# Performance work log

Measured on AMD Instinct MI355X. Metric: run time of the kernel, lower is better.

Reference implementation:

```python
import jax, jax.numpy as jnp
import numpy as np

N_NODES = 5000
N_EDGES = 50000
HIDDEN = 64
EDGE_DIM = 16


def setup_inputs() -> dict:
    key = jax.random.key(0)
    ks = jax.random.split(key, 8)
    d = HIDDEN
    h = jax.random.normal(ks[0], (N_NODES, d), dtype=jnp.float32)
    edge_index = jax.random.randint(ks[1], (2, N_EDGES), 0, N_NODES, dtype=jnp.int64)
    edge_features = jax.random.normal(ks[2], (N_EDGES, EDGE_DIM), dtype=jnp.float32)
    # edge-network MLP: Linear(edge_dim, d) -> ReLU -> Linear(d, d*d)
    W1 = jax.random.normal(ks[3], (EDGE_DIM, d), dtype=jnp.float32) * (1.0 / np.sqrt(EDGE_DIM))
    b1 = jnp.zeros((d,), dtype=jnp.float32)
    W2 = jax.random.normal(ks[4], (d, d * d), dtype=jnp.float32) * (1.0 / np.sqrt(d))
    b2 = jnp.zeros((d * d,), dtype=jnp.float32)
    # GRUCell params (torch layout: rows = [reset; update; new])
    W_ih = jax.random.normal(ks[5], (3 * d, d), dtype=jnp.float32) * (1.0 / np.sqrt(d))
    W_hh = jax.random.normal(ks[6], (3 * d, d), dtype=jnp.float32) * (1.0 / np.sqrt(d))
    b_ih = jnp.zeros((3 * d,), dtype=jnp.float32)
    b_hh = jnp.zeros((3 * d,), dtype=jnp.float32)
    return {"h": h, "edge_index": edge_index, "edge_features": edge_features,
            "W1": W1, "b1": b1, "W2": W2, "b2": b2,
            "W_ih": W_ih, "W_hh": W_hh, "b_ih": b_ih, "b_hh": b_hh}


def reference(h, edge_index, edge_features, W1, b1, W2, b2, W_ih, W_hh, b_ih, b_hh):
    n_nodes, d = h.shape
    src, tgt = edge_index[0], edge_index[1]
    # 1) gather sender states
    h_w = h[src]  # (E, d)
    # 2-3) edge MLP -> per-edge transformation matrices (E, d, d)
    A = jax.nn.relu(edge_features @ W1 + b1) @ W2 + b2
    A = A.reshape(-1, d, d)
    # 4) per-edge matvec messages
    msg = jnp.einsum('eij,ej->ei', A, h_w)  # (E, d)
    # 5) scatter-sum aggregation per target node
    m = jax.ops.segment_sum(msg, tgt, num_segments=n_nodes)  # (N, d)
    # 6) GRUCell(m, h) - torch semantics
    gi = m @ W_ih.T + b_ih   # (N, 3d)
    gh = h @ W_hh.T + b_hh   # (N, 3d)
    i_r, i_z, i_n = jnp.split(gi, 3, axis=-1)
    h_r, h_z, h_n = jnp.split(gh, 3, axis=-1)
    r = jax.nn.sigmoid(i_r + h_r)
    z = jax.nn.sigmoid(i_z + h_z)
    n = jnp.tanh(i_n + r * h_n)
    h_new = (1.0 - z) * n + z * h
    return h_new
```

## Files before the change

kernel.cpp:

```cpp
#include <hip/hip_runtime.h>
#include <math.h>

#define N_NODES 5000
#define N_EDGES 50000
#define NPAD 5008
#define KP 4224
#define KSPLIT 3
#define POISON_I ((int)0xAAAAAAAAu)

typedef _Float16 f16x8 __attribute__((ext_vector_type(8)));
typedef _Float16 f16x2 __attribute__((ext_vector_type(2)));
typedef float    f32x4 __attribute__((ext_vector_type(4)));

static __device__ __forceinline__ f32x4 mfma16f(f16x8 a, f16x8 b, f32x4 c) {
    return __builtin_amdgcn_mfma_f32_16x16x32_f16(a, b, c, 0, 0, 0);
}

__global__ void prep_kernel(const float* __restrict__ W2, const float* __restrict__ b2,
                            const float* __restrict__ Wih, const float* __restrict__ Whh,
                            const int* __restrict__ ei,
                            _Float16* __restrict__ Br, float* __restrict__ WihT,
                            float* __restrict__ WhhT, int* __restrict__ cnt) {
    int g = blockIdx.x * 256 + threadIdx.x;
    if (g < 33792) {
        int nt = g / 8448, rem = g - nt * 8448;
        int ks = rem >> 6, lane = rem & 63;
        int lo = lane & 15, q = lane >> 4;
        int i = nt * 16 + lo, kap0 = ks * 32 + q * 8;
        f16x8 v;
#pragma unroll
        for (int p = 0; p < 8; ++p) {
            int kap = kap0 + p;
            int k2 = kap >> 7, rem2 = kap & 127;
            int j = rem2 >> 1, k = k2 * 2 + (rem2 & 1);
            float x = 0.f;
            if (k < 64) x = W2[(size_t)k * 4096 + i * 64 + j];
            else if (k == 64) x = b2[i * 64 + j];
            v[p] = (_Float16)x;
        }
        *(f16x8*)(Br + (size_t)g * 8) = v;
        return;
    }
    g -= 33792;
    if (g < 24576) {
        int which = g >= 12288;
        int tt = which ? g - 12288 : g;
        int row = tt >> 6, j = tt & 63;
        (which ? WhhT : WihT)[j * 192 + row] = (which ? Whh : Wih)[tt];
        return;
    }
    g -= 24576;
    if (g < N_EDGES) atomicAdd(&cnt[ei[N_EDGES + g]], 1);
}

__global__ __launch_bounds__(1024) void scan_kernel(const int* __restrict__ cnt,
                                                    int* __restrict__ off,
                                                    int* __restrict__ cur) {
    __shared__ int s[1024];
    int tid = threadIdx.x;
    int base = tid * 5;
    int loc[5]; int sum = 0;
#pragma unroll
    for (int q = 0; q < 5; ++q) {
        int v = (base + q < N_NODES) ? (cnt[base + q] - POISON_I) : 0;
        loc[q] = sum; sum += v;
    }
    s[tid] = sum; __syncthreads();
    for (int d = 1; d < 1024; d <<= 1) {
        int v = (tid >= d) ? s[tid - d] : 0;
        __syncthreads();
        s[tid] += v;
        __syncthreads();
    }
    int excl = (tid > 0) ? s[tid - 1] : 0;
#pragma unroll
    for (int q = 0; q < 5; ++q)
        if (base + q < N_NODES) { off[base + q] = excl + loc[q]; cur[base + q] = excl + loc[q]; }
    if (tid == 1023) off[N_NODES] = excl + sum;
}

__global__ void scatter_kernel(const int* __restrict__ ei, int* __restrict__ cur,
                               int* __restrict__ srcp, int* __restrict__ eidp) {
    int e = blockIdx.x * 256 + threadIdx.x;
    if (e < N_EDGES) {
        int q = atomicAdd(&cur[ei[N_EDGES + e]], 1);
        srcp[q] = ei[e];
        eidp[q] = e;
    }
}

__global__ __launch_bounds__(256) void hbuild_kernel(const int* __restrict__ toff,
                                                     const int* __restrict__ srcp,
                                                     const int* __restrict__ eidp,
                                                     const float* __restrict__ ef,
                                                     const float* __restrict__ W1,
                                                     const float* __restrict__ b1,
                                                     const float* __restrict__ h,
                                                     _Float16* __restrict__ H) {
    __shared__ float tls[16][64];
    __shared__ float hls[16][64];
    int tid = threadIdx.x, kc = tid >> 6, lane = tid & 63;
    int v = blockIdx.x;
    float acc[16];
#pragma unroll
    for (int k = 0; k < 16; ++k) acc[k] = 0.f;
    float acc64 = 0.f;
    int s0 = 0, s1 = 0;
    if (v < N_NODES) { s0 = toff[v]; s1 = toff[v + 1]; }
    float w1c[16];
#pragma unroll
    for (int k = 0; k < 16; ++k) w1c[k] = W1[k * 64 + lane];
    float b1l = b1[lane];
    for (int tb = s0; tb < s1; tb += 16) {
        int tcnt = s1 - tb; if (tcnt > 16) tcnt = 16;
        int eidx[4], sidx[4];
#pragma unroll
        for (int r = 0; r < 4; ++r) {
            int idx = kc * 4 + r;
            if (idx < tcnt) {
                eidx[r] = eidp[tb + idx];
                sidx[r] = srcp[tb + idx];
            }
        }
#pragma unroll
        for (int r = 0; r < 4; ++r) {
            int idx = kc * 4 + r;
            if (idx < tcnt) {
                hls[idx][lane] = h[(size_t)sidx[r] * 64 + lane];
                const float* efr = ef + (size_t)eidx[r] * 16;
                float tacc = b1l;
#pragma unroll
                for (int k = 0; k < 16; ++k) tacc += efr[k] * w1c[k];
                tls[idx][lane] = fmaxf(tacc, 0.f);
            }
        }
        __syncthreads();
        int q = 0;
        for (; q + 1 < tcnt; q += 2) {
            float hv0 = hls[q][lane];
            float hv1 = hls[q + 1][lane];
            const float4* t0 = (const float4*)&tls[q][kc * 16];
            const float4* t1 = (const float4*)&tls[q + 1][kc * 16];
#pragma unroll
            for (int b = 0; b < 4; ++b) {
                float4 a = t0[b], c = t1[b];
                acc[b * 4 + 0] += a.x * hv0; acc[b * 4 + 0] += c.x * hv1;
                acc[b * 4 + 1] += a.y * hv0; acc[b * 4 + 1] += c.y * hv1;
                acc[b * 4 + 2] += a.z * hv0; acc[b * 4 + 2] += c.z * hv1;
                acc[b * 4 + 3] += a.w * hv0; acc[b * 4 + 3] += c.w * hv1;
            }
            acc64 += hv0 + hv1;
        }
        if (q < tcnt) {
            float hv = hls[q][lane];
            const float4* t0 = (const float4*)&tls[q][kc * 16];
#pragma unroll
            for (int b = 0; b < 4; ++b) {
                float4 a = t0[b];
                acc[b * 4 + 0] += a.x * hv;
                acc[b * 4 + 1] += a.y * hv;
                acc[b * 4 + 2] += a.z * hv;
                acc[b * 4 + 3] += a.w * hv;
            }
            acc64 += hv;
        }
        __syncthreads();
    }
    _Float16* Hv = H + (size_t)v * KP;
#pragma unroll
    for (int p = 0; p < 8; ++p) {
        f16x2 pv = { (_Float16)acc[p * 2], (_Float16)acc[p * 2 + 1] };
        *(f16x2*)(Hv + (kc * 8 + p) * 128 + lane * 2) = pv;
    }
    if (kc == 3) {
        f16x2 pv = { (_Float16)acc64, (_Float16)0.f };
        *(f16x2*)(Hv + 32 * 128 + lane * 2) = pv;
    }
}

__global__ __launch_bounds__(256) void gemm_part(const _Float16* __restrict__ H,
                                                 const _Float16* __restrict__ Br,
                                                 float* __restrict__ gp) {
    __shared__ _Float16 As[2][16 * 136];
    int tid = threadIdx.x, w = tid >> 6, lane = tid & 63;
    int lo = lane & 15, q = lane >> 4;
    int m0 = blockIdx.x * 16;
    int ksp = blockIdx.y;
    int ar = tid >> 4, ac = (tid & 15) * 8;
    const _Float16* Ag = H + (size_t)(m0 + ar) * KP + ksp * 1408 + ac;
    f32x4 acc = {0.f, 0.f, 0.f, 0.f};
    f16x8 pf = *(const f16x8*)(Ag);
    *(f16x8*)(&As[0][ar * 136 + ac]) = pf;
    __syncthreads();
    for (int c = 0; c < 11; ++c) {
        if (c + 1 < 11) pf = *(const f16x8*)(Ag + (size_t)(c + 1) * 128);
        const _Float16* Arow = &As[c & 1][lo * 136];
        int ksg = (ksp * 11 + c) * 4;
#pragma unroll
        for (int ks = 0; ks < 4; ++ks) {
            f16x8 a = *(const f16x8*)(Arow + ks * 32 + q * 8);
            f16x8 b = *(const f16x8*)(Br + ((size_t)((w * 132 + ksg + ks) * 64 + lane)) * 8);
            acc = mfma16f(a, b, acc);
        }
        if (c + 1 < 11) *(f16x8*)(&As[(c + 1) & 1][ar * 136 + ac]) = pf;
        __syncthreads();
    }
    float* gpo = gp + (size_t)ksp * NPAD * 64;
    int row4 = q * 4;
#pragma unroll
    for (int g = 0; g < 4; ++g)
        gpo[(size_t)(m0 + row4 + g) * 64 + w * 16 + lo] = acc[g];
}

__global__ void gru_kernel(const float* __restrict__ gp,
                           const float* __restrict__ h,
                           const float* __restrict__ WihT,
                           const float* __restrict__ WhhT,
                           const float* __restrict__ bih,
                           const float* __restrict__ bhh,
                           float* __restrict__ out) {
    int w = threadIdx.x >> 6, lane = threadIdx.x & 63;
    int n = blockIdx.x * 4 + w;
    int i = lane;
    float ir = bih[i], iz = bih[64 + i], inn = bih[128 + i];
    float hr = bhh[i], hz = bhh[64 + i], hn = bhh[128 + i];
    const float4* g0 = (const float4*)(gp + (size_t)n * 64);
    const float4* g1 = (const float4*)(gp + (size_t)NPAD * 64 + (size_t)n * 64);
    const float4* g2 = (const float4*)(gp + (size_t)2 * NPAD * 64 + (size_t)n * 64);
    const float4* hnp = (const float4*)(h + (size_t)n * 64);
#pragma unroll 4
    for (int qb = 0; qb < 16; ++qb) {
        float4 a = g0[qb], b = g1[qb], c = g2[qb];
        float4 hv = hnp[qb];
        float mj[4] = {a.x + b.x + c.x, a.y + b.y + c.y,
                       a.z + b.z + c.z, a.w + b.w + c.w};
        float hj[4] = {hv.x, hv.y, hv.z, hv.w};
#pragma unroll
        for (int u = 0; u < 4; ++u) {
            int j = qb * 4 + u;
            const float* wi = WihT + j * 192;
            const float* wh = WhhT + j * 192;
            ir  += mj[u] * wi[i];
            iz  += mj[u] * wi[64 + i];
            inn += mj[u] * wi[128 + i];
            hr  += hj[u] * wh[i];
            hz  += hj[u] * wh[64 + i];
            hn  += hj[u] * wh[128 + i];
        }
    }
    float hval = h[(size_t)n * 64 + i];
    float r = 1.f / (1.f + expf(-(ir + hr)));
    float z = 1.f / (1.f + expf(-(iz + hz)));
    float nn = tanhf(inn + r * hn);
    out[n * 64 + i] = (1.f - z) * nn + z * hval;
}

extern "C" void kernel_launch(void* const* d_in, const int* in_sizes, int n_in,
                              void* d_out, int out_size, void* d_ws, size_t ws_size,
                              hipStream_t stream) {
    const float* h   = (const float*)d_in[0];
    const int*   ei  = (const int*)d_in[1];
    const float* ef  = (const float*)d_in[2];
    const float* W1  = (const float*)d_in[3];
    const float* b1  = (const float*)d_in[4];
    const float* W2  = (const float*)d_in[5];
    const float* b2  = (const float*)d_in[6];
    const float* Wih = (const float*)d_in[7];
    const float* Whh = (const float*)d_in[8];
    const float* bih = (const float*)d_in[9];
    const float* bhh = (const float*)d_in[10];
    float* out = (float*)d_out;

    _Float16* H    = (_Float16*)d_ws;
    _Float16* Br   = H + (size_t)NPAD * KP;
    float*    WihT = (float*)(Br + 270336);
    float*    WhhT = WihT + 12288;
    float*    gp   = WhhT + 12288;
    int*      cnt  = (int*)(gp + (size_t)3 * NPAD * 64);
    int*      toff = cnt + N_NODES;
    int*      cur  = toff + N_NODES + 1;
    int*      srcp = cur + N_NODES;
    int*      eidp = srcp + N_EDGES;

    prep_kernel<<<424, 256, 0, stream>>>(W2, b2, Wih, Whh, ei, Br, WihT, WhhT, cnt);
    scan_kernel<<<1, 1024, 0, stream>>>(cnt, toff, cur);
    scatter_kernel<<<196, 256, 0, stream>>>(ei, cur, srcp, eidp);
    hbuild_kernel<<<NPAD, 256, 0, stream>>>(toff, srcp, eidp, ef, W1, b1, h, H);
    gemm_part<<<dim3(313, KSPLIT), 256, 0, stream>>>(H, Br, gp);
    gru_kernel<<<1250, 256, 0, stream>>>(gp, h, WihT, WhhT, bih, bhh, out);
}
```

Before: 152.0 us.

## Move GRU gate GEMMs onto fp16 MFMA and store hbuild edge activations as fp16

The scalar fp32 GRU kernel is replaced by an MFMA version. Each block handles 16 nodes, stages m and h as fp16 in LDS, multiplies them against pre-packed fp16 W_ih/W_hh fragments built in prep_kernel, and applies the gate nonlinearities from an LDS buffer. Separately, hbuild stores the ReLU edge-MLP activations as fp16 in shared memory, halving LDS traffic for the outer-product accumulation. Both changes lower precision of the GRU inputs and the edge activations to fp16, which adds rounding error.

Result: faster. 135.3 us (-11.0%).

```diff
diff --git a/kernel.cpp b/kernel.cpp
--- a/kernel.cpp
+++ b/kernel.cpp
@@ -19,8 +19,8 @@
 __global__ void prep_kernel(const float* __restrict__ W2, const float* __restrict__ b2,
                             const float* __restrict__ Wih, const float* __restrict__ Whh,
                             const int* __restrict__ ei,
-                            _Float16* __restrict__ Br, float* __restrict__ WihT,
-                            float* __restrict__ WhhT, int* __restrict__ cnt) {
+                            _Float16* __restrict__ Br, _Float16* __restrict__ Bg2,
+                            int* __restrict__ cnt) {
     int g = blockIdx.x * 256 + threadIdx.x;
     if (g < 33792) {
         int nt = g / 8448, rem = g - nt * 8448;
@@ -42,14 +42,19 @@
         return;
     }
     g -= 33792;
-    if (g < 24576) {
-        int which = g >= 12288;
-        int tt = which ? g - 12288 : g;
-        int row = tt >> 6, j = tt & 63;
-        (which ? WhhT : WihT)[j * 192 + row] = (which ? Whh : Wih)[tt];
+    if (g < 3072) {
+        int ct = g >> 7, ks = (g >> 6) & 1, lane = g & 63;
+        int lo = lane & 15, q = lane >> 4;
+        const float* src = (ct < 12) ? Wih : Whh;
+        int r = ((ct < 12) ? ct : ct - 12) * 16 + lo;
+        int j0 = ks * 32 + q * 8;
+        f16x8 v;
+#pragma unroll
+        for (int p = 0; p < 8; ++p) v[p] = (_Float16)src[r * 64 + j0 + p];
+        *(f16x8*)(Bg2 + (size_t)g * 8) = v;
         return;
     }
-    g -= 24576;
+    g -= 3072;
     if (g < N_EDGES) atomicAdd(&cnt[ei[N_EDGES + g]], 1);
 }
 
@@ -97,7 +102,7 @@
                                                      const float* __restrict__ b1,
                                                      const float* __restrict__ h,
                                                      _Float16* __restrict__ H) {
-    __shared__ float tls[16][64];
+    __shared__ _Float16 tls[16][64];
     __shared__ float hls[16][64];
     int tid = threadIdx.x, kc = tid >> 6, lane = tid & 63;
     int v = blockIdx.x;
@@ -131,7 +136,7 @@
                 float tacc = b1l;
 #pragma unroll
                 for (int k = 0; k < 16; ++k) tacc += efr[k] * w1c[k];
-                tls[idx][lane] = fmaxf(tacc, 0.f);
+                tls[idx][lane] = (_Float16)fmaxf(tacc, 0.f);
             }
         }
         __syncthreads();
@@ -139,28 +144,25 @@
         for (; q + 1 < tcnt; q += 2) {
             float hv0 = hls[q][lane];
             float hv1 = hls[q + 1][lane];
-            const float4* t0 = (const float4*)&tls[q][kc * 16];
-            const float4* t1 = (const float4*)&tls[q + 1][kc * 16];
-#pragma unroll
-            for (int b = 0; b < 4; ++b) {
-                float4 a = t0[b], c = t1[b];
-                acc[b * 4 + 0] += a.x * hv0; acc[b * 4 + 0] += c.x * hv1;
-                acc[b * 4 + 1] += a.y * hv0; acc[b * 4 + 1] += c.y * hv1;
-                acc[b * 4 + 2] += a.z * hv0; acc[b * 4 + 2] += c.z * hv1;
-                acc[b * 4 + 3] += a.w * hv0; acc[b * 4 + 3] += c.w * hv1;
+            const f16x8* t0 = (const f16x8*)&tls[q][kc * 16];
+            const f16x8* t1 = (const f16x8*)&tls[q + 1][kc * 16];
+            f16x8 a0 = t0[0], a1 = t0[1];
+            f16x8 c0 = t1[0], c1 = t1[1];
+#pragma unroll
+            for (int p = 0; p < 8; ++p) {
+                acc[p]     += (float)a0[p] * hv0 + (float)c0[p] * hv1;
+                acc[8 + p] += (float)a1[p] * hv0 + (float)c1[p] * hv1;
             }
             acc64 += hv0 + hv1;
         }
         if (q < tcnt) {
             float hv = hls[q][lane];
-            const float4* t0 = (const float4*)&tls[q][kc * 16];
-#pragma unroll
-            for (int b = 0; b < 4; ++b) {
-                float4 a = t0[b];
-                acc[b * 4 + 0] += a.x * hv;
-                acc[b * 4 + 1] += a.y * hv;
-                acc[b * 4 + 2] += a.z * hv;
-                acc[b * 4 + 3] += a.w * hv;
+            const f16x8* t0 = (const f16x8*)&tls[q][kc * 16];
+            f16x8 a0 = t0[0], a1 = t0[1];
+#pragma unroll
+            for (int p = 0; p < 8; ++p) {
+                acc[p]     += (float)a0[p] * hv;
+                acc[8 + p] += (float)a1[p] * hv;
             }
             acc64 += hv;
         }
@@ -212,47 +214,80 @@
         gpo[(size_t)(m0 + row4 + g) * 64 + w * 16 + lo] = acc[g];
 }
 
-__global__ void gru_kernel(const float* __restrict__ gp,
-                           const float* __restrict__ h,
-                           const float* __restrict__ WihT,
-                           const float* __restrict__ WhhT,
-                           const float* __restrict__ bih,
-                           const float* __restrict__ bhh,
-                           float* __restrict__ out) {
-    int w = threadIdx.x >> 6, lane = threadIdx.x & 63;
-    int n = blockIdx.x * 4 + w;
+__global__ __launch_bounds__(256) void gru_mfma(const float* __restrict__ gp,
+                                                const float* __restrict__ h,
+                                                const _Float16* __restrict__ Bg2,
+                                                const float* __restrict__ bih,
+                                                const float* __restrict__ bhh,
+                                                float* __restrict__ out) {
+    __shared__ _Float16 mls[16 * 72];
+    __shared__ _Float16 hls[16 * 72];
+    __shared__ float gbuf[16 * 385];
+    int tid = threadIdx.x, w = tid >> 6, lane = tid & 63;
+    int lo = lane & 15, q = lane >> 4;
+    int m0 = blockIdx.x * 16;
+#pragma unroll
+    for (int r = 0; r < 4; ++r) {
+        int idx = r * 256 + tid, nl = idx >> 6, j = idx & 63;
+        int n = m0 + nl;
+        float mv = 0.f, hv = 0.f;
+        if (n < N_NODES) {
+            mv = gp[(size_t)n * 64 + j] + gp[(size_t)NPAD * 64 + (size_t)n * 64 + j]
+               + gp[(size_t)2 * NPAD * 64 + (size_t)n * 64 + j];
+            hv = h[(size_t)n * 64 + j];
+        }
+        mls[nl * 72 + j] = (_Float16)mv;
+        hls[nl * 72 + j] = (_Float16)hv;
+    }
+    __syncthreads();
+    f16x8 am[2], ah[2];
+    am[0] = *(const f16x8*)&mls[lo * 72 + q * 8];
+    am[1] = *(const f16x8*)&mls[lo * 72 + 32 + q * 8];
+    ah[0] = *(const f16x8*)&hls[lo * 72 + q * 8];
+    ah[1] = *(const f16x8*)&hls[lo * 72 + 32 + q * 8];
+    f32x4 zero4 = {0.f, 0.f, 0.f, 0.f};
+    f32x4 acc[6] = {zero4, zero4, zero4, zero4, zero4, zero4};
+#pragma unroll
+    for (int j = 0; j < 3; ++j) {
+        int ctg = w + 4 * j;
+        int cth = 12 + w + 4 * j;
+#pragma unroll
+        for (int ks = 0; ks < 2; ++ks) {
+            f16x8 bg = *(const f16x8*)(Bg2 + ((size_t)((ctg * 2 + ks) * 64 + lane)) * 8);
+            f16x8 bh = *(const f16x8*)(Bg2 + ((size_t)((cth * 2 + ks) * 64 + lane)) * 8);
+            acc[j]     = mfma16f(am[ks], bg, acc[j]);
+            acc[3 + j] = mfma16f(ah[ks], bh, acc[3 + j]);
+        }
+    }
+#pragma unroll
+    for (int j = 0; j < 3; ++j) {
+        int colg = (w + 4 * j) * 16 + lo;
+        int colh = 192 + colg;
+#pragma unroll
+        for (int g = 0; g < 4; ++g) {
+            gbuf[(q * 4 + g) * 385 + colg] = acc[j][g];
+            gbuf[(q * 4 + g) * 385 + colh] = acc[3 + j][g];
+        }
+    }
+    __syncthreads();
     int i = lane;
-    float ir = bih[i], iz = bih[64 + i], inn = bih[128 + i];
-    float hr = bhh[i], hz = bhh[64 + i], hn = bhh[128 + i];
-    const float4* g0 = (const float4*)(gp + (size_t)n * 64);
-    const float4* g1 = (const float4*)(gp + (size_t)NPAD * 64 + (size_t)n * 64);
-    const float4* g2 = (const float4*)(gp + (size_t)2 * NPAD * 64 + (size_t)n * 64);
-    const float4* hnp = (const float4*)(h + (size_t)n * 64);
-#pragma unroll 4
-    for (int qb = 0; qb < 16; ++qb) {
-        float4 a = g0[qb], b = g1[qb], c = g2[qb];
-        float4 hv = hnp[qb];
-        float mj[4] = {a.x + b.x + c.x, a.y + b.y + c.y,
-                       a.z + b.z + c.z, a.w + b.w + c.w};
-        float hj[4] = {hv.x, hv.y, hv.z, hv.w};
-#pragma unroll
-        for (int u = 0; u < 4; ++u) {
-            int j = qb * 4 + u;
-            const float* wi = WihT + j * 192;
-            const float* wh = WhhT + j * 192;
-            ir  += mj[u] * wi[i];
-            iz  += mj[u] * wi[64 + i];
-            inn += mj[u] * wi[128 + i];
-            hr  += hj[u] * wh[i];
-            hz  += hj[u] * wh[64 + i];
-            hn  += hj[u] * wh[128 + i];
-        }
-    }
-    float hval = h[(size_t)n * 64 + i];
-    float r = 1.f / (1.f + expf(-(ir + hr)));
-    float z = 1.f / (1.f + expf(-(iz + hz)));
-    float nn = tanhf(inn + r * hn);
-    out[n * 64 + i] = (1.f - z) * nn + z * hval;
+#pragma unroll
+    for (int u = 0; u < 4; ++u) {
+        int nl = w * 4 + u, n = m0 + nl;
+        if (n >= N_NODES) continue;
+        const float* gb = gbuf + nl * 385;
+        float ir  = gb[i]       + bih[i];
+        float iz  = gb[64 + i]  + bih[64 + i];
+        float inn = gb[128 + i] + bih[128 + i];
+        float hr  = gb[192 + i] + bhh[i];
+        float hz  = gb[256 + i] + bhh[64 + i];
+        float hn  = gb[320 + i] + bhh[128 + i];
+        float hval = h[(size_t)n * 64 + i];
+        float r = 1.f / (1.f + expf(-(ir + hr)));
+        float z = 1.f / (1.f + expf(-(iz + hz)));
+        float nn = tanhf(inn + r * hn);
+        out[n * 64 + i] = (1.f - z) * nn + z * hval;
+    }
 }
 
 extern "C" void kernel_launch(void* const* d_in, const int* in_sizes, int n_in,
@@ -273,19 +308,18 @@
 
     _Float16* H    = (_Float16*)d_ws;
     _Float16* Br   = H + (size_t)NPAD * KP;
-    float*    WihT = (float*)(Br + 270336);
-    float*    WhhT = WihT + 12288;
-    float*    gp   = WhhT + 12288;
+    _Float16* Bg2  = Br + 270336;
+    float*    gp   = (float*)(Bg2 + 24576);
     int*      cnt  = (int*)(gp + (size_t)3 * NPAD * 64);
     int*      toff = cnt + N_NODES;
     int*      cur  = toff + N_NODES + 1;
     int*      srcp = cur + N_NODES;
     int*      eidp = srcp + N_EDGES;
 
-    prep_kernel<<<424, 256, 0, stream>>>(W2, b2, Wih, Whh, ei, Br, WihT, WhhT, cnt);
+    prep_kernel<<<340, 256, 0, stream>>>(W2, b2, Wih, Whh, ei, Br, Bg2, cnt);
     scan_kernel<<<1, 1024, 0, stream>>>(cnt, toff, cur);
     scatter_kernel<<<196, 256, 0, stream>>>(ei, cur, srcp, eidp);
     hbuild_kernel<<<NPAD, 256, 0, stream>>>(toff, srcp, eidp, ef, W1, b1, h, H);
     gemm_part<<<dim3(313, KSPLIT), 256, 0, stream>>>(H, Br, gp);
-    gru_kernel<<<1250, 256, 0, stream>>>(gp, h, WihT, WhhT, bih, bhh, out);
-}
+    gru_mfma<<<313, 256, 0, stream>>>(gp, h, Bg2, bih, bhh, out);
+}
```
